# Kernel tuning notes

Measured on AMD Instinct MI355X. Metric: run time of the kernel, lower is better.

## Reference

```python
import math
import jax, jax.numpy as jnp
import numpy as np

N_GRAPHS = 400
N_PER = 50
N = N_GRAPHS * N_PER          # 20000 nodes
K = 12                        # k_neighbors
E = N * K                     # 240000 edges
ND = 128                      # node_dim
TD = 128                      # time_dim
LD = 128                      # latent_dim
SD = 32                       # species_emb_dim
L = 4                         # num_layers


def _lin(key, fi, fo):
    return (jax.random.normal(key, (fi, fo), dtype=jnp.float32) / np.sqrt(fi)).astype(jnp.float32)


def setup_inputs() -> dict:
    rng = np.random.default_rng(0)
    coords = (rng.standard_normal((N_GRAPHS, N_PER, 3)) * 3.0).astype(np.float32)
    # exact kNN per graph (loop=False): dst = center node, src = neighbor
    d = ((coords[:, :, None, :] - coords[:, None, :, :]) ** 2).sum(-1)  # [G, n, n]
    ii = np.arange(N_PER)
    d[:, ii, ii] = np.inf
    nbr = np.argpartition(d, K, axis=-1)[:, :, :K]                      # [G, n, K]
    base = (np.arange(N_GRAPHS) * N_PER)[:, None, None]
    edge_src = (nbr + base).reshape(-1).astype(np.int64)
    edge_dst = (np.broadcast_to(ii[None, :, None], (N_GRAPHS, N_PER, K)) + base).reshape(-1).astype(np.int64)
    batch_indices = np.repeat(np.arange(N_GRAPHS), N_PER).astype(np.int64)

    key = jax.random.key(0)
    ks = jax.random.split(key, 32)
    inp = {
        'z_nodes': jax.random.normal(ks[0], (N, LD), dtype=jnp.float32),
        't': jax.random.uniform(ks[1], (N_GRAPHS,), dtype=jnp.float32) * 1000.0,
        'cart_coords': jnp.asarray(coords.reshape(N, 3)),
        'species': jax.random.randint(ks[2], (N,), 1, 119),
        'batch_indices': jnp.asarray(batch_indices),
        'edge_src': jnp.asarray(edge_src),
        'edge_dst': jnp.asarray(edge_dst),
        # parameters
        'species_emb': jax.random.normal(ks[3], (119, SD), dtype=jnp.float32),
        'tm_W1': _lin(ks[4], TD, 2 * TD), 'tm_b1': jnp.zeros((2 * TD,), jnp.float32),
        'tm_W2': _lin(ks[5], 2 * TD, TD), 'tm_b2': jnp.zeros((TD,), jnp.float32),
        'ne_W': _lin(ks[6], LD + SD, ND), 'ne_b': jnp.zeros((ND,), jnp.float32),
        'eW1': jnp.stack([_lin(jax.random.fold_in(ks[7], l), 2 * ND + 1 + TD, ND) for l in range(L)]),
        'eb1': jnp.zeros((L, ND), jnp.float32),
        'eW2': jnp.stack([_lin(jax.random.fold_in(ks[8], l), ND, ND) for l in range(L)]),
        'eb2': jnp.zeros((L, ND), jnp.float32),
        'cW1': jnp.stack([_lin(jax.random.fold_in(ks[9], l), ND, ND) for l in range(L)]),
        'cb1': jnp.zeros((L, ND), jnp.float32),
        'cW2': jnp.stack([_lin(jax.random.fold_in(ks[10], l), ND, 1) for l in range(L)]),
        'nW1': jnp.stack([_lin(jax.random.fold_in(ks[11], l), 2 * ND + TD, ND) for l in range(L)]),
        'nb1': jnp.zeros((L, ND), jnp.float32),
        'nW2': jnp.stack([_lin(jax.random.fold_in(ks[12], l), ND, ND) for l in range(L)]),
        'nb2': jnp.zeros((L, ND), jnp.float32),
    }
    return inp


def reference(z_nodes, t, cart_coords, species, batch_indices, edge_src, edge_dst,
              species_emb, tm_W1, tm_b1, tm_W2, tm_b2, ne_W, ne_b,
              eW1, eb1, eW2, eb2, cW1, cb1, cW2, nW1, nb1, nW2, nb2):
    silu = jax.nn.silu
    # sinusoidal time embedding + time MLP
    half = TD // 2
    freqs = jnp.exp(jnp.arange(half, dtype=jnp.float32) * (-math.log(10000.0) / (half - 1)))
    ang = t[:, None] * freqs[None, :]                     # [G, half]
    temb = jnp.concatenate([jnp.sin(ang), jnp.cos(ang)], axis=-1)
    temb = silu(temb @ tm_W1 + tm_b1) @ tm_W2 + tm_b2     # [G, TD]
    t_nodes = temb[batch_indices]                         # [N, TD]

    sp = species_emb[species]                             # [N, SD]
    h = jnp.concatenate([z_nodes, sp], axis=-1) @ ne_W + ne_b  # [N, ND]

    diff = cart_coords[edge_src] - cart_coords[edge_dst]  # [E, 3]
    dist_sq = jnp.sum(diff * diff, axis=-1, keepdims=True)  # [E, 1]
    dist = jnp.sqrt(dist_sq + 1e-8)
    t_edges = t_nodes[edge_src]                           # [E, TD]

    n = h.shape[0]
    total_shift = jnp.zeros_like(cart_coords)
    for l in range(L):
        edge_in = jnp.concatenate([h[edge_src], h[edge_dst], dist_sq, t_edges], axis=-1)
        m = silu(edge_in @ eW1[l] + eb1[l])
        m = silu(m @ eW2[l] + eb2[l])                     # [E, ND]
        gate = silu(m @ cW1[l] + cb1[l]) @ cW2[l]         # [E, 1]
        shift = diff / dist * gate                        # [E, 3]
        total_shift = total_shift + jax.ops.segment_sum(shift, edge_dst, num_segments=n)
        m_i = jax.ops.segment_sum(m, edge_dst, num_segments=n)  # [N, ND]
        node_in = jnp.concatenate([h, m_i, t_nodes], axis=-1)
        h = h + (silu(node_in @ nW1[l] + nb1[l]) @ nW2[l] + nb2[l])
    return (total_shift, h)
```

## Files before the change

### kernel.cpp

```cpp
#include <hip/hip_runtime.h>
#include <math.h>

#define GN 400
#define NPER 50
#define NN 20000
#define LL 4

typedef __attribute__((ext_vector_type(8))) short short8;
typedef __attribute__((ext_vector_type(4))) float f32x4;

__device__ __forceinline__ float fast_rcp(float x) {
#if __has_builtin(__builtin_amdgcn_rcpf)
  return __builtin_amdgcn_rcpf(x);
#else
  return 1.0f / x;
#endif
}
__device__ __forceinline__ float silu_f(float x) {
  return x * fast_rcp(1.0f + __expf(-x));
}
__device__ __forceinline__ unsigned short f2bu(float f) {
  unsigned int u = __float_as_uint(f);
  unsigned int r = (u + 0x7fffu + ((u >> 16) & 1u)) >> 16;
  return (unsigned short)r;
}
__device__ __forceinline__ unsigned int pack2bf(float lo, float hi) {
  return (unsigned int)f2bu(lo) | ((unsigned int)f2bu(hi) << 16);
}
__device__ __forceinline__ float bhi(unsigned int u) { return __uint_as_float(u & 0xffff0000u); }
__device__ __forceinline__ float blo(unsigned int u) { return __uint_as_float(u << 16); }

__device__ __forceinline__ short8 pack8(const float* v) {
  union { unsigned int u[4]; short8 s; } t;
  t.u[0] = pack2bf(v[0], v[1]);
  t.u[1] = pack2bf(v[2], v[3]);
  t.u[2] = pack2bf(v[4], v[5]);
  t.u[3] = pack2bf(v[6], v[7]);
  return t.s;
}

__global__ __launch_bounds__(128) void time_kernel(
    const float* __restrict__ t,
    const float* __restrict__ tm_W1, const float* __restrict__ tm_b1,
    const float* __restrict__ tm_W2, const float* __restrict__ tm_b2,
    const float* __restrict__ eW1, const float* __restrict__ eb1,
    const float* __restrict__ nW1, const float* __restrict__ nb1,
    float* __restrict__ temb, float* __restrict__ tE, float* __restrict__ tN)
{
  int g = blockIdx.x;
  int j = threadIdx.x;
  __shared__ float x[128];
  __shared__ float hid[256];
  __shared__ float te[128];
  float tv = t[g];
  if (j < 64) {
    float f = __expf((float)j * (-9.210340371976184f / 63.0f));
    float a = tv * f;
    x[j] = sinf(a);
    x[j + 64] = cosf(a);
  }
  __syncthreads();
  for (int o = j; o < 256; o += 128) {
    float acc = tm_b1[o];
    for (int k = 0; k < 128; ++k) acc = fmaf(x[k], tm_W1[k * 256 + o], acc);
    hid[o] = silu_f(acc);
  }
  __syncthreads();
  {
    float acc = tm_b2[j];
    for (int k = 0; k < 256; ++k) acc = fmaf(hid[k], tm_W2[k * 128 + j], acc);
    te[j] = acc;
    temb[g * 128 + j] = acc;
  }
  __syncthreads();
  for (int l = 0; l < LL; ++l) {
    const float* W = eW1 + (l * 385 + 257) * 128;
    float acc = eb1[l * 128 + j];
    for (int k = 0; k < 128; ++k) acc = fmaf(te[k], W[k * 128 + j], acc);
    tE[(l * GN + g) * 128 + j] = acc;
    const float* Wn = nW1 + (l * 384 + 256) * 128;
    float acc2 = nb1[l * 128 + j];
    for (int k = 0; k < 128; ++k) acc2 = fmaf(te[k], Wn[k * 128 + j], acc2);
    tN[(l * GN + g) * 128 + j] = acc2;
  }
}

__global__ __launch_bounds__(256) void prep_transpose(
    const float* __restrict__ eW1, const float* __restrict__ eW2,
    const float* __restrict__ cW1, const float* __restrict__ nW1,
    const float* __restrict__ nW2, const float* __restrict__ ne_W,
    unsigned short* __restrict__ eABt, unsigned short* __restrict__ eW2t,
    unsigned short* __restrict__ cW1t, unsigned short* __restrict__ nW1t,
    unsigned short* __restrict__ nW2t, unsigned short* __restrict__ ne_Wt)
{
  __shared__ float tile[32][33];
  int j = blockIdx.y;
  const float* src;
  unsigned short* dst;
  int dstride = 128, Kj = 128;
  if (j < 28) {
    int l = j / 7, m = j % 7;
    switch (m) {
      case 0: src = eW1 + (l * 385 + 0) * 128;   dst = eABt + l * 256 * 128;             break;
      case 1: src = eW1 + (l * 385 + 128) * 128; dst = eABt + l * 256 * 128 + 128 * 128; break;
      case 2: src = eW2 + l * 16384;             dst = eW2t + l * 16384;                 break;
      case 3: src = cW1 + l * 16384;             dst = cW1t + l * 16384;                 break;
      case 4: src = nW1 + (l * 384 + 0) * 128;   dst = nW1t + l * 128 * 256; dstride = 256; break;
      case 5: src = nW1 + (l * 384 + 128) * 128; dst = nW1t + l * 128 * 256 + 128; dstride = 256; break;
      default: src = nW2 + l * 16384;            dst = nW2t + l * 16384;                 break;
    }
  } else {
    src = ne_W; dst = ne_Wt; dstride = 160; Kj = 160;
  }
  int gx = blockIdx.x;
  int tk = (gx % 5) * 32;
  int tn = (gx / 5) * 32;
  if (tk >= Kj) return;
  int ti = threadIdx.x >> 5, tj = threadIdx.x & 31;
#pragma unroll
  for (int p = 0; p < 4; ++p) {
    int i = ti + p * 8;
    tile[i][tj] = src[(tk + i) * 128 + tn + tj];
  }
  __syncthreads();
#pragma unroll
  for (int p = 0; p < 4; ++p) {
    int i = ti + p * 8;
    dst[(tn + i) * dstride + tk + tj] = f2bu(tile[tj][i]);
  }
}

__global__ __launch_bounds__(64) void edge_mfma(
    const unsigned short* __restrict__ hAB,
    const float* __restrict__ coords, const int* __restrict__ edge_src,
    const float* __restrict__ eW1,
    const unsigned short* __restrict__ eW2t, const float* __restrict__ eb2,
    const unsigned short* __restrict__ cW1t, const float* __restrict__ cb1,
    const float* __restrict__ cW2, const float* __restrict__ tE,
    unsigned short* __restrict__ m_i, float* __restrict__ shift_out,
    int l, int addflag)
{
  __shared__ unsigned short mbuf[48 * 136];
  __shared__ float sdir[48 * 4];
  __shared__ float sgate[48];

  int l6 = threadIdx.x;
  int e16 = l6 & 15, q = l6 >> 4;
  int nbase = blockIdx.x * 4;
  int ebase = blockIdx.x * 48;

  const unsigned short* eW2t_l = eW2t + l * 16384;
  const unsigned short* cW1t_l = cW1t + l * 16384;
  const float* eb2_l = eb2 + l * 128;
  const float* cb1_l = cb1 + l * 128;
  const float* cW2_l = cW2 + l * 128;
  const float* tE_l = tE + l * GN * 128;
  const float* wd = eW1 + (l * 385 + 256) * 128;

  int ssrc[3], sdst[3];
  float sds[3];
#pragma unroll
  for (int grp = 0; grp < 3; ++grp) {
    int eloc = grp * 16 + e16;
    int e = ebase + eloc;
    int src = edge_src[e];
    src = min(max(src, 0), NN - 1);
    int dst = nbase + eloc / 12;
    float dx = coords[src * 3 + 0] - coords[dst * 3 + 0];
    float dy = coords[src * 3 + 1] - coords[dst * 3 + 1];
    float dz = coords[src * 3 + 2] - coords[dst * 3 + 2];
    float ds = dx * dx + dy * dy + dz * dz;
    float rinv = 1.0f / sqrtf(ds + 1e-8f);
    if (q == 0) {
      sdir[eloc * 4 + 0] = dx * rinv;
      sdir[eloc * 4 + 1] = dy * rinv;
      sdir[eloc * 4 + 2] = dz * rinv;
    }
    ssrc[grp] = src; sdst[grp] = dst; sds[grp] = ds;
  }

  short8 bfr[3][4];
#pragma unroll
  for (int grp = 0; grp < 3; ++grp) {
    int g = sdst[grp] / NPER;
    float ds = sds[grp];
#pragma unroll
    for (int kc = 0; kc < 4; ++kc) {
      int k0 = kc * 32 + q * 8;
      uint4 ua = *(const uint4*)(hAB + ssrc[grp] * 256 + k0);
      uint4 ub = *(const uint4*)(hAB + sdst[grp] * 256 + 128 + k0);
      float4 w0 = *(const float4*)(wd + k0);
      float4 w1 = *(const float4*)(wd + k0 + 4);
      float4 t0 = *(const float4*)(tE_l + g * 128 + k0);
      float4 t1 = *(const float4*)(tE_l + g * 128 + k0 + 4);
      float v[8];
      v[0] = silu_f(blo(ua.x) + blo(ub.x) + ds * w0.x + t0.x);
      v[1] = silu_f(bhi(ua.x) + bhi(ub.x) + ds * w0.y + t0.y);
      v[2] = silu_f(blo(ua.y) + blo(ub.y) + ds * w0.z + t0.z);
      v[3] = silu_f(bhi(ua.y) + bhi(ub.y) + ds * w0.w + t0.w);
      v[4] = silu_f(blo(ua.z) + blo(ub.z) + ds * w1.x + t1.x);
      v[5] = silu_f(bhi(ua.z) + bhi(ub.z) + ds * w1.y + t1.y);
      v[6] = silu_f(blo(ua.w) + blo(ub.w) + ds * w1.z + t1.z);
      v[7] = silu_f(bhi(ua.w) + bhi(ub.w) + ds * w1.w + t1.w);
      bfr[grp][kc] = pack8(v);
    }
  }

#pragma unroll
  for (int mt = 0; mt < 8; ++mt) {
    short8 af[4];
#pragma unroll
    for (int kc = 0; kc < 4; ++kc)
      af[kc] = *(const short8*)(eW2t_l + (mt * 16 + e16) * 128 + kc * 32 + q * 8);
    f32x4 acc[3] = {(f32x4){0,0,0,0}, (f32x4){0,0,0,0}, (f32x4){0,0,0,0}};
#pragma unroll
    for (int kc = 0; kc < 4; ++kc) {
#pragma unroll
      for (int grp = 0; grp < 3; ++grp)
        acc[grp] = __builtin_amdgcn_mfma_f32_16x16x32_bf16(af[kc], bfr[grp][kc], acc[grp], 0, 0, 0);
    }
    float4 b4 = *(const float4*)(eb2_l + mt * 16 + q * 4);
#pragma unroll
    for (int grp = 0; grp < 3; ++grp) {
      float v0 = silu_f(acc[grp][0] + b4.x);
      float v1 = silu_f(acc[grp][1] + b4.y);
      float v2 = silu_f(acc[grp][2] + b4.z);
      float v3 = silu_f(acc[grp][3] + b4.w);
      uint2 p;
      p.x = pack2bf(v0, v1);
      p.y = pack2bf(v2, v3);
      *(uint2*)&mbuf[(grp * 16 + e16) * 136 + mt * 16 + q * 4] = p;
    }
  }
  __syncthreads();

  short8 af2[3][4];
#pragma unroll
  for (int grp = 0; grp < 3; ++grp)
#pragma unroll
    for (int kc = 0; kc < 4; ++kc)
      af2[grp][kc] = *(const short8*)&mbuf[(grp * 16 + e16) * 136 + kc * 32 + q * 8];

  float gp[3][4] = {{0,0,0,0},{0,0,0,0},{0,0,0,0}};
#pragma unroll
  for (int ct = 0; ct < 8; ++ct) {
    short8 bf[4];
#pragma unroll
    for (int kc = 0; kc < 4; ++kc)
      bf[kc] = *(const short8*)(cW1t_l + (ct * 16 + e16) * 128 + kc * 32 + q * 8);
    f32x4 acc[3] = {(f32x4){0,0,0,0}, (f32x4){0,0,0,0}, (f32x4){0,0,0,0}};
#pragma unroll
    for (int kc = 0; kc < 4; ++kc) {
#pragma unroll
      for (int grp = 0; grp < 3; ++grp)
        acc[grp] = __builtin_amdgcn_mfma_f32_16x16x32_bf16(af2[grp][kc], bf[kc], acc[grp], 0, 0, 0);
    }
    float cb = cb1_l[ct * 16 + e16];
    float c2 = cW2_l[ct * 16 + e16];
#pragma unroll
    for (int grp = 0; grp < 3; ++grp)
#pragma unroll
      for (int r = 0; r < 4; ++r)
        gp[grp][r] += silu_f(acc[grp][r] + cb) * c2;
  }
#pragma unroll
  for (int grp = 0; grp < 3; ++grp)
#pragma unroll
    for (int r = 0; r < 4; ++r) {
      float v = gp[grp][r];
      v += __shfl_xor(v, 1);
      v += __shfl_xor(v, 2);
      v += __shfl_xor(v, 4);
      v += __shfl_xor(v, 8);
      if (e16 == 0) sgate[grp * 16 + q * 4 + r] = v;
    }
  __syncthreads();

  {
    int nl = q, c8 = e16 * 8;
    float s[8] = {0,0,0,0,0,0,0,0};
#pragma unroll
    for (int r = 0; r < 12; ++r) {
      uint4 u = *(const uint4*)&mbuf[(nl * 12 + r) * 136 + c8];
      s[0] += blo(u.x); s[1] += bhi(u.x);
      s[2] += blo(u.y); s[3] += bhi(u.y);
      s[4] += blo(u.z); s[5] += bhi(u.z);
      s[6] += blo(u.w); s[7] += bhi(u.w);
    }
    uint4 o;
    o.x = pack2bf(s[0], s[1]); o.y = pack2bf(s[2], s[3]);
    o.z = pack2bf(s[4], s[5]); o.w = pack2bf(s[6], s[7]);
    *(uint4*)(m_i + (nbase + nl) * 128 + c8) = o;
  }
  if (l6 < 12) {
    int nl = l6 / 3, c = l6 - nl * 3;
    float s = 0.f;
#pragma unroll
    for (int r = 0; r < 12; ++r) {
      int e = nl * 12 + r;
      s = fmaf(sdir[e * 4 + c], sgate[e], s);
    }
    int n = nbase + nl;
    if (addflag) shift_out[n * 3 + c] += s;
    else         shift_out[n * 3 + c] = s;
  }
}

__global__ __launch_bounds__(64) void node_mfma(
    float* __restrict__ h, const unsigned short* __restrict__ m_i,
    const unsigned short* __restrict__ nW1t_l, const unsigned short* __restrict__ nW2t_l,
    const float* __restrict__ nb2_l, const float* __restrict__ tN_l,
    const unsigned short* __restrict__ eABt_next, unsigned short* __restrict__ hAB,
    int has_c)
{
  __shared__ unsigned short z1buf[16 * 136];
  __shared__ unsigned short hbuf[16 * 136];
  int l6 = threadIdx.x, e16 = l6 & 15, q = l6 >> 4;
  int row = blockIdx.x * 16 + e16;
  int g = row / NPER;

  short8 bfh[8];
#pragma unroll
  for (int kc = 0; kc < 8; ++kc) {
    int k0 = kc * 32 + q * 8;
    if (k0 < 128) {
      float4 f0 = *(const float4*)(h + row * 128 + k0);
      float4 f1 = *(const float4*)(h + row * 128 + k0 + 4);
      float v[8] = {f0.x, f0.y, f0.z, f0.w, f1.x, f1.y, f1.z, f1.w};
      bfh[kc] = pack8(v);
    } else {
      bfh[kc] = *(const short8*)(m_i + row * 128 + (k0 - 128));
    }
  }
#pragma unroll
  for (int mt = 0; mt < 8; ++mt) {
    short8 af[8];
#pragma unroll
    for (int kc = 0; kc < 8; ++kc)
      af[kc] = *(const short8*)(nW1t_l + (mt * 16 + e16) * 256 + kc * 32 + q * 8);
    f32x4 acc = (f32x4){0,0,0,0};
#pragma unroll
    for (int kc = 0; kc < 8; ++kc)
      acc = __builtin_amdgcn_mfma_f32_16x16x32_bf16(af[kc], bfh[kc], acc, 0, 0, 0);
    float4 tv = *(const float4*)(tN_l + g * 128 + mt * 16 + q * 4);
    float v0 = silu_f(acc[0] + tv.x);
    float v1 = silu_f(acc[1] + tv.y);
    float v2 = silu_f(acc[2] + tv.z);
    float v3 = silu_f(acc[3] + tv.w);
    uint2 p; p.x = pack2bf(v0, v1); p.y = pack2bf(v2, v3);
    *(uint2*)&z1buf[e16 * 136 + mt * 16 + q * 4] = p;
  }
  __syncthreads();

  short8 zf[4];
#pragma unroll
  for (int kc = 0; kc < 4; ++kc)
    zf[kc] = *(const short8*)&z1buf[e16 * 136 + kc * 32 + q * 8];
#pragma unroll
  for (int mt = 0; mt < 8; ++mt) {
    short8 af[4];
#pragma unroll
    for (int kc = 0; kc < 4; ++kc)
      af[kc] = *(const short8*)(nW2t_l + (mt * 16 + e16) * 128 + kc * 32 + q * 8);
    f32x4 acc = (f32x4){0,0,0,0};
#pragma unroll
    for (int kc = 0; kc < 4; ++kc)
      acc = __builtin_amdgcn_mfma_f32_16x16x32_bf16(af[kc], zf[kc], acc, 0, 0, 0);
    float4 hv = *(const float4*)(h + row * 128 + mt * 16 + q * 4);
    float4 b4 = *(const float4*)(nb2_l + mt * 16 + q * 4);
    float4 o;
    o.x = hv.x + acc[0] + b4.x;
    o.y = hv.y + acc[1] + b4.y;
    o.z = hv.z + acc[2] + b4.z;
    o.w = hv.w + acc[3] + b4.w;
    *(float4*)(h + row * 128 + mt * 16 + q * 4) = o;
    uint2 p; p.x = pack2bf(o.x, o.y); p.y = pack2bf(o.z, o.w);
    *(uint2*)&hbuf[e16 * 136 + mt * 16 + q * 4] = p;
  }
  if (has_c) {
    __syncthreads();
    short8 hf[4];
#pragma unroll
    for (int kc = 0; kc < 4; ++kc)
      hf[kc] = *(const short8*)&hbuf[e16 * 136 + kc * 32 + q * 8];
#pragma unroll
    for (int mt = 0; mt < 16; ++mt) {
      short8 af[4];
#pragma unroll
      for (int kc = 0; kc < 4; ++kc)
        af[kc] = *(const short8*)(eABt_next + (mt * 16 + e16) * 128 + kc * 32 + q * 8);
      f32x4 acc = (f32x4){0,0,0,0};
#pragma unroll
      for (int kc = 0; kc < 4; ++kc)
        acc = __builtin_amdgcn_mfma_f32_16x16x32_bf16(af[kc], hf[kc], acc, 0, 0, 0);
      uint2 p; p.x = pack2bf(acc[0], acc[1]); p.y = pack2bf(acc[2], acc[3]);
      *(uint2*)(hAB + row * 256 + mt * 16 + q * 4) = p;
    }
  }
}

__global__ __launch_bounds__(64) void encoder_mfma(
    const float* __restrict__ z, const int* __restrict__ species,
    const float* __restrict__ species_emb,
    const unsigned short* __restrict__ ne_Wt, const float* __restrict__ ne_b,
    const unsigned short* __restrict__ eABt0,
    float* __restrict__ h, unsigned short* __restrict__ hAB)
{
  __shared__ unsigned short hbuf[16 * 136];
  int l6 = threadIdx.x, e16 = l6 & 15, q = l6 >> 4;
  int row = blockIdx.x * 16 + e16;
  int sp = species[row];
  sp = min(max(sp, 0), 118);

  short8 bfh[5];
#pragma unroll
  for (int kc = 0; kc < 5; ++kc) {
    int k0 = kc * 32 + q * 8;
    const float* src = (k0 < 128) ? (z + row * 128 + k0)
                                  : (species_emb + sp * 32 + (k0 - 128));
    float4 f0 = *(const float4*)src;
    float4 f1 = *(const float4*)(src + 4);
    float v[8] = {f0.x, f0.y, f0.z, f0.w, f1.x, f1.y, f1.z, f1.w};
    bfh[kc] = pack8(v);
  }
#pragma unroll
  for (int mt = 0; mt < 8; ++mt) {
    short8 af[5];
#pragma unroll
    for (int kc = 0; kc < 5; ++kc)
      af[kc] = *(const short8*)(ne_Wt + (mt * 16 + e16) * 160 + kc * 32 + q * 8);
    f32x4 acc = (f32x4){0,0,0,0};
#pragma unroll
    for (int kc = 0; kc < 5; ++kc)
      acc = __builtin_amdgcn_mfma_f32_16x16x32_bf16(af[kc], bfh[kc], acc, 0, 0, 0);
    float4 b4 = *(const float4*)(ne_b + mt * 16 + q * 4);
    float4 o;
    o.x = acc[0] + b4.x; o.y = acc[1] + b4.y;
    o.z = acc[2] + b4.z; o.w = acc[3] + b4.w;
    *(float4*)(h + row * 128 + mt * 16 + q * 4) = o;
    uint2 p; p.x = pack2bf(o.x, o.y); p.y = pack2bf(o.z, o.w);
    *(uint2*)&hbuf[e16 * 136 + mt * 16 + q * 4] = p;
  }
  __syncthreads();
  short8 hf[4];
#pragma unroll
  for (int kc = 0; kc < 4; ++kc)
    hf[kc] = *(const short8*)&hbuf[e16 * 136 + kc * 32 + q * 8];
#pragma unroll
  for (int mt = 0; mt < 16; ++mt) {
    short8 af[4];
#pragma unroll
    for (int kc = 0; kc < 4; ++kc)
      af[kc] = *(const short8*)(eABt0 + (mt * 16 + e16) * 128 + kc * 32 + q * 8);
    f32x4 acc = (f32x4){0,0,0,0};
#pragma unroll
    for (int kc = 0; kc < 4; ++kc)
      acc = __builtin_amdgcn_mfma_f32_16x16x32_bf16(af[kc], hf[kc], acc, 0, 0, 0);
    uint2 p; p.x = pack2bf(acc[0], acc[1]); p.y = pack2bf(acc[2], acc[3]);
    *(uint2*)(hAB + row * 256 + mt * 16 + q * 4) = p;
  }
}

extern "C" void kernel_launch(void* const* d_in, const int* in_sizes, int n_in,
                              void* d_out, int out_size, void* d_ws, size_t ws_size,
                              hipStream_t stream)
{
  const float* z_nodes     = (const float*)d_in[0];
  const float* t           = (const float*)d_in[1];
  const float* coords      = (const float*)d_in[2];
  const int*   species     = (const int*)d_in[3];
  const int*   edge_src    = (const int*)d_in[5];
  const float* species_emb = (const float*)d_in[7];
  const float* tm_W1 = (const float*)d_in[8];
  const float* tm_b1 = (const float*)d_in[9];
  const float* tm_W2 = (const float*)d_in[10];
  const float* tm_b2 = (const float*)d_in[11];
  const float* ne_W  = (const float*)d_in[12];
  const float* ne_b  = (const float*)d_in[13];
  const float* eW1   = (const float*)d_in[14];
  const float* eb1   = (const float*)d_in[15];
  const float* eW2   = (const float*)d_in[16];
  const float* eb2   = (const float*)d_in[17];
  const float* cW1   = (const float*)d_in[18];
  const float* cb1   = (const float*)d_in[19];
  const float* cW2   = (const float*)d_in[20];
  const float* nW1   = (const float*)d_in[21];
  const float* nb1   = (const float*)d_in[22];
  const float* nW2   = (const float*)d_in[23];
  const float* nb2   = (const float*)d_in[24];

  char* wsb = (char*)d_ws;
  float* temb = (float*)(wsb + 0);
  float* tEb  = (float*)(wsb + 204800);
  float* tNb  = (float*)(wsb + 1024000);
  unsigned short* hAB  = (unsigned short*)(wsb + 1843200);
  unsigned short* m_i  = (unsigned short*)(wsb + 12083200);
  unsigned short* eABt = (unsigned short*)(wsb + 17203200);
  unsigned short* eW2t = (unsigned short*)(wsb + 17465344);
  unsigned short* cW1t = (unsigned short*)(wsb + 17596416);
  unsigned short* nW1t = (unsigned short*)(wsb + 17727488);
  unsigned short* nW2t = (unsigned short*)(wsb + 17989632);
  unsigned short* ne_Wt= (unsigned short*)(wsb + 18120704);

  float* outp  = (float*)d_out;
  float* shift = outp;
  float* h     = outp + 60000;

  time_kernel<<<GN, 128, 0, stream>>>(t, tm_W1, tm_b1, tm_W2, tm_b2,
                                      eW1, eb1, nW1, nb1, temb, tEb, tNb);
  prep_transpose<<<dim3(20, 29), 256, 0, stream>>>(eW1, eW2, cW1, nW1, nW2, ne_W,
                                                   eABt, eW2t, cW1t, nW1t, nW2t, ne_Wt);
  encoder_mfma<<<NN / 16, 64, 0, stream>>>(z_nodes, species, species_emb,
                                           ne_Wt, ne_b, eABt, h, hAB);
  for (int l = 0; l < LL; ++l) {
    edge_mfma<<<NN / 4, 64, 0, stream>>>(hAB, coords, edge_src, eW1,
                                         eW2t, eb2, cW1t, cb1, cW2, tEb,
                                         m_i, shift, l, (l > 0) ? 1 : 0);
    int has_c = (l < LL - 1) ? 1 : 0;
    node_mfma<<<NN / 16, 64, 0, stream>>>(h, m_i,
                                          nW1t + l * 128 * 256, nW2t + l * 16384,
                                          nb2 + l * 128, tNb + l * GN * 128,
                                          has_c ? (eABt + (l + 1) * 256 * 128) : eABt,
                                          hAB, has_c);
  }
}
```

Before: 550.3 us.

## Use two-wave blocks and cheaper bf16 packing across edge, node and encoder kernels

Edge blocks now hold two independent wavefronts, each with its own shared-memory slice, and the block-wide barriers are replaced by block memory fences. Node and encoder kernels split their output tiles across two waves so each wave does half the MFMA tiles. bf16 packing moves from round-to-nearest-even to add-and-perm rounding. The aim is higher occupancy, less barrier cost and fewer ALU ops. The risks are that intra-wave LDS reuse without a barrier depends on lockstep wavefront execution, that rounding changes slightly, and that the node and encoder kernels each do more redundant B-fragment loads per wave.

```diff
diff --git a/kernel.cpp b/kernel.cpp
--- a/kernel.cpp
+++ b/kernel.cpp
@@ -25,7 +25,13 @@
   return (unsigned short)r;
 }
 __device__ __forceinline__ unsigned int pack2bf(float lo, float hi) {
-  return (unsigned int)f2bu(lo) | ((unsigned int)f2bu(hi) << 16);
+  unsigned int a = __float_as_uint(lo) + 0x8000u;
+  unsigned int b = __float_as_uint(hi) + 0x8000u;
+#if __has_builtin(__builtin_amdgcn_perm)
+  return __builtin_amdgcn_perm(b, a, 0x07060302);
+#else
+  return (b & 0xffff0000u) | (a >> 16);
+#endif
 }
 __device__ __forceinline__ float bhi(unsigned int u) { return __uint_as_float(u & 0xffff0000u); }
 __device__ __forceinline__ float blo(unsigned int u) { return __uint_as_float(u << 16); }
@@ -130,7 +136,7 @@
   }
 }
 
-__global__ __launch_bounds__(64) void edge_mfma(
+__global__ __launch_bounds__(128) void edge_mfma(
     const unsigned short* __restrict__ hAB,
     const float* __restrict__ coords, const int* __restrict__ edge_src,
     const float* __restrict__ eW1,
@@ -140,14 +146,19 @@
     unsigned short* __restrict__ m_i, float* __restrict__ shift_out,
     int l, int addflag)
 {
-  __shared__ unsigned short mbuf[48 * 136];
-  __shared__ float sdir[48 * 4];
-  __shared__ float sgate[48];
-
-  int l6 = threadIdx.x;
+  __shared__ unsigned short mbuf[2][48 * 136];
+  __shared__ float sdir[2][48 * 4];
+  __shared__ float sgate[2][48];
+
+  int tid = threadIdx.x;
+  int wv = tid >> 6;
+  int l6 = tid & 63;
   int e16 = l6 & 15, q = l6 >> 4;
-  int nbase = blockIdx.x * 4;
-  int ebase = blockIdx.x * 48;
+  int nbase = blockIdx.x * 8 + wv * 4;
+  int ebase = nbase * 12;
+  unsigned short* mb = mbuf[wv];
+  float* sd = sdir[wv];
+  float* sg = sgate[wv];
 
   const unsigned short* eW2t_l = eW2t + l * 16384;
   const unsigned short* cW1t_l = cW1t + l * 16384;
@@ -172,9 +183,9 @@
     float ds = dx * dx + dy * dy + dz * dz;
     float rinv = 1.0f / sqrtf(ds + 1e-8f);
     if (q == 0) {
-      sdir[eloc * 4 + 0] = dx * rinv;
-      sdir[eloc * 4 + 1] = dy * rinv;
-      sdir[eloc * 4 + 2] = dz * rinv;
+      sd[eloc * 4 + 0] = dx * rinv;
+      sd[eloc * 4 + 1] = dy * rinv;
+      sd[eloc * 4 + 2] = dz * rinv;
     }
     ssrc[grp] = src; sdst[grp] = dst; sds[grp] = ds;
   }
@@ -229,17 +240,17 @@
       uint2 p;
       p.x = pack2bf(v0, v1);
       p.y = pack2bf(v2, v3);
-      *(uint2*)&mbuf[(grp * 16 + e16) * 136 + mt * 16 + q * 4] = p;
-    }
-  }
-  __syncthreads();
+      *(uint2*)&mb[(grp * 16 + e16) * 136 + mt * 16 + q * 4] = p;
+    }
+  }
+  __threadfence_block();
 
   short8 af2[3][4];
 #pragma unroll
   for (int grp = 0; grp < 3; ++grp)
 #pragma unroll
     for (int kc = 0; kc < 4; ++kc)
-      af2[grp][kc] = *(const short8*)&mbuf[(grp * 16 + e16) * 136 + kc * 32 + q * 8];
+      af2[grp][kc] = *(const short8*)&mb[(grp * 16 + e16) * 136 + kc * 32 + q * 8];
 
   float gp[3][4] = {{0,0,0,0},{0,0,0,0},{0,0,0,0}};
 #pragma unroll
@@ -272,16 +283,16 @@
       v += __shfl_xor(v, 2);
       v += __shfl_xor(v, 4);
       v += __shfl_xor(v, 8);
-      if (e16 == 0) sgate[grp * 16 + q * 4 + r] = v;
-    }
-  __syncthreads();
+      if (e16 == 0) sg[grp * 16 + q * 4 + r] = v;
+    }
+  __threadfence_block();
 
   {
     int nl = q, c8 = e16 * 8;
     float s[8] = {0,0,0,0,0,0,0,0};
 #pragma unroll
     for (int r = 0; r < 12; ++r) {
-      uint4 u = *(const uint4*)&mbuf[(nl * 12 + r) * 136 + c8];
+      uint4 u = *(const uint4*)&mb[(nl * 12 + r) * 136 + c8];
       s[0] += blo(u.x); s[1] += bhi(u.x);
       s[2] += blo(u.y); s[3] += bhi(u.y);
       s[4] += blo(u.z); s[5] += bhi(u.z);
@@ -298,7 +309,7 @@
 #pragma unroll
     for (int r = 0; r < 12; ++r) {
       int e = nl * 12 + r;
-      s = fmaf(sdir[e * 4 + c], sgate[e], s);
+      s = fmaf(sd[e * 4 + c], sg[e], s);
     }
     int n = nbase + nl;
     if (addflag) shift_out[n * 3 + c] += s;
@@ -306,7 +317,7 @@
   }
 }
 
-__global__ __launch_bounds__(64) void node_mfma(
+__global__ __launch_bounds__(128) void node_mfma(
     float* __restrict__ h, const unsigned short* __restrict__ m_i,
     const unsigned short* __restrict__ nW1t_l, const unsigned short* __restrict__ nW2t_l,
     const float* __restrict__ nb2_l, const float* __restrict__ tN_l,
@@ -315,7 +326,9 @@
 {
   __shared__ unsigned short z1buf[16 * 136];
   __shared__ unsigned short hbuf[16 * 136];
-  int l6 = threadIdx.x, e16 = l6 & 15, q = l6 >> 4;
+  int tid = threadIdx.x;
+  int wv = tid >> 6, l6 = tid & 63;
+  int e16 = l6 & 15, q = l6 >> 4;
   int row = blockIdx.x * 16 + e16;
   int g = row / NPER;
 
@@ -333,7 +346,8 @@
     }
   }
 #pragma unroll
-  for (int mt = 0; mt < 8; ++mt) {
+  for (int mi = 0; mi < 4; ++mi) {
+    int mt = wv * 4 + mi;
     short8 af[8];
 #pragma unroll
     for (int kc = 0; kc < 8; ++kc)
@@ -357,7 +371,8 @@
   for (int kc = 0; kc < 4; ++kc)
     zf[kc] = *(const short8*)&z1buf[e16 * 136 + kc * 32 + q * 8];
 #pragma unroll
-  for (int mt = 0; mt < 8; ++mt) {
+  for (int mi = 0; mi < 4; ++mi) {
+    int mt = wv * 4 + mi;
     short8 af[4];
 #pragma unroll
     for (int kc = 0; kc < 4; ++kc)
@@ -384,7 +399,8 @@
     for (int kc = 0; kc < 4; ++kc)
       hf[kc] = *(const short8*)&hbuf[e16 * 136 + kc * 32 + q * 8];
 #pragma unroll
-    for (int mt = 0; mt < 16; ++mt) {
+    for (int mi = 0; mi < 8; ++mi) {
+      int mt = wv * 8 + mi;
       short8 af[4];
 #pragma unroll
       for (int kc = 0; kc < 4; ++kc)
@@ -399,7 +415,7 @@
   }
 }
 
-__global__ __launch_bounds__(64) void encoder_mfma(
+__global__ __launch_bounds__(128) void encoder_mfma(
     const float* __restrict__ z, const int* __restrict__ species,
     const float* __restrict__ species_emb,
     const unsigned short* __restrict__ ne_Wt, const float* __restrict__ ne_b,
@@ -407,7 +423,9 @@
     float* __restrict__ h, unsigned short* __restrict__ hAB)
 {
   __shared__ unsigned short hbuf[16 * 136];
-  int l6 = threadIdx.x, e16 = l6 & 15, q = l6 >> 4;
+  int tid = threadIdx.x;
+  int wv = tid >> 6, l6 = tid & 63;
+  int e16 = l6 & 15, q = l6 >> 4;
   int row = blockIdx.x * 16 + e16;
   int sp = species[row];
   sp = min(max(sp, 0), 118);
@@ -424,7 +442,8 @@
     bfh[kc] = pack8(v);
   }
 #pragma unroll
-  for (int mt = 0; mt < 8; ++mt) {
+  for (int mi = 0; mi < 4; ++mi) {
+    int mt = wv * 4 + mi;
     short8 af[5];
 #pragma unroll
     for (int kc = 0; kc < 5; ++kc)
@@ -447,7 +466,8 @@
   for (int kc = 0; kc < 4; ++kc)
     hf[kc] = *(const short8*)&hbuf[e16 * 136 + kc * 32 + q * 8];
 #pragma unroll
-  for (int mt = 0; mt < 16; ++mt) {
+  for (int mi = 0; mi < 8; ++mi) {
+    int mt = wv * 8 + mi;
     short8 af[4];
 #pragma unroll
     for (int kc = 0; kc < 4; ++kc)
@@ -510,17 +530,17 @@
                                       eW1, eb1, nW1, nb1, temb, tEb, tNb);
   prep_transpose<<<dim3(20, 29), 256, 0, stream>>>(eW1, eW2, cW1, nW1, nW2, ne_W,
                                                    eABt, eW2t, cW1t, nW1t, nW2t, ne_Wt);
-  encoder_mfma<<<NN / 16, 64, 0, stream>>>(z_nodes, species, species_emb,
-                                           ne_Wt, ne_b, eABt, h, hAB);
+  encoder_mfma<<<NN / 16, 128, 0, stream>>>(z_nodes, species, species_emb,
+                                            ne_Wt, ne_b, eABt, h, hAB);
   for (int l = 0; l < LL; ++l) {
-    edge_mfma<<<NN / 4, 64, 0, stream>>>(hAB, coords, edge_src, eW1,
-                                         eW2t, eb2, cW1t, cb1, cW2, tEb,
-                                         m_i, shift, l, (l > 0) ? 1 : 0);
+    edge_mfma<<<NN / 8, 128, 0, stream>>>(hAB, coords, edge_src, eW1,
+                                          eW2t, eb2, cW1t, cb1, cW2, tEb,
+                                          m_i, shift, l, (l > 0) ? 1 : 0);
     int has_c = (l < LL - 1) ? 1 : 0;
-    node_mfma<<<NN / 16, 64, 0, stream>>>(h, m_i,
-                                          nW1t + l * 128 * 256, nW2t + l * 16384,
-                                          nb2 + l * 128, tNb + l * GN * 128,
-                                          has_c ? (eABt + (l + 1) * 256 * 128) : eABt,
-                                          hAB, has_c);
-  }
-}
+    node_mfma<<<NN / 16, 128, 0, stream>>>(h, m_i,
+                                           nW1t + l * 128 * 256, nW2t + l * 16384,
+                                           nb2 + l * 128, tNb + l * GN * 128,
+                                           has_c ? (eABt + (l + 1) * 256 * 128) : eABt,
+                                           hAB, has_c);
+  }
+}
```

Result: no change. 554.8 us (+0.8%).

## Process eight nodes per edge block to reuse weight fragments; cheaper bf16 packing

Applied to the files above, without the earlier changes.

Each edge_mfma block now handles two 48-edge chunks (8 destination nodes), so each eW2/cW1 weight fragment loaded from global memory feeds twice as many MFMAs. The grid is halved and shared memory is doubled. Separately, pack2bf now rounds half-up and packs the two values with a byte-permute instruction instead of round-to-nearest-even. This cuts instruction count but changes the rounding slightly. The larger register footprint (bfr, af2 and accumulators all doubled) risks spills or lower occupancy.

```diff
diff --git a/kernel.cpp b/kernel.cpp
--- a/kernel.cpp
+++ b/kernel.cpp
@@ -25,7 +25,13 @@
   return (unsigned short)r;
 }
 __device__ __forceinline__ unsigned int pack2bf(float lo, float hi) {
-  return (unsigned int)f2bu(lo) | ((unsigned int)f2bu(hi) << 16);
+  unsigned int a = __float_as_uint(lo) + 0x8000u;
+  unsigned int b = __float_as_uint(hi) + 0x8000u;
+#if __has_builtin(__builtin_amdgcn_perm)
+  return __builtin_amdgcn_perm(b, a, 0x07060302);
+#else
+  return (b & 0xffff0000u) | (a >> 16);
+#endif
 }
 __device__ __forceinline__ float bhi(unsigned int u) { return __uint_as_float(u & 0xffff0000u); }
 __device__ __forceinline__ float blo(unsigned int u) { return __uint_as_float(u << 16); }
@@ -140,14 +146,13 @@
     unsigned short* __restrict__ m_i, float* __restrict__ shift_out,
     int l, int addflag)
 {
-  __shared__ unsigned short mbuf[48 * 136];
-  __shared__ float sdir[48 * 4];
-  __shared__ float sgate[48];
+  __shared__ unsigned short mbuf[2][48 * 136];
+  __shared__ float sdir[2][48 * 4];
+  __shared__ float sgate[2][48];
 
   int l6 = threadIdx.x;
   int e16 = l6 & 15, q = l6 >> 4;
-  int nbase = blockIdx.x * 4;
-  int ebase = blockIdx.x * 48;
+  int nbase0 = blockIdx.x * 8;
 
   const unsigned short* eW2t_l = eW2t + l * 16384;
   const unsigned short* cW1t_l = cW1t + l * 16384;
@@ -157,38 +162,45 @@
   const float* tE_l = tE + l * GN * 128;
   const float* wd = eW1 + (l * 385 + 256) * 128;
 
-  int ssrc[3], sdst[3];
-  float sds[3];
+  int ssrc[2][3], sdst[2][3];
+  float sds[2][3];
+#pragma unroll
+  for (int c = 0; c < 2; ++c) {
+    int nbase = nbase0 + c * 4;
+    int ebase = nbase * 12;
+#pragma unroll
+    for (int grp = 0; grp < 3; ++grp) {
+      int eloc = grp * 16 + e16;
+      int e = ebase + eloc;
+      int src = edge_src[e];
+      src = min(max(src, 0), NN - 1);
+      int dst = nbase + eloc / 12;
+      float dx = coords[src * 3 + 0] - coords[dst * 3 + 0];
+      float dy = coords[src * 3 + 1] - coords[dst * 3 + 1];
+      float dz = coords[src * 3 + 2] - coords[dst * 3 + 2];
+      float ds = dx * dx + dy * dy + dz * dz;
+      float rinv = 1.0f / sqrtf(ds + 1e-8f);
+      if (q == 0) {
+        sdir[c][eloc * 4 + 0] = dx * rinv;
+        sdir[c][eloc * 4 + 1] = dy * rinv;
+        sdir[c][eloc * 4 + 2] = dz * rinv;
+      }
+      ssrc[c][grp] = src; sdst[c][grp] = dst; sds[c][grp] = ds;
+    }
+  }
+
+  short8 bfr[2][3][4];
+#pragma unroll
+  for (int c = 0; c < 2; ++c)
 #pragma unroll
   for (int grp = 0; grp < 3; ++grp) {
-    int eloc = grp * 16 + e16;
-    int e = ebase + eloc;
-    int src = edge_src[e];
-    src = min(max(src, 0), NN - 1);
-    int dst = nbase + eloc / 12;
-    float dx = coords[src * 3 + 0] - coords[dst * 3 + 0];
-    float dy = coords[src * 3 + 1] - coords[dst * 3 + 1];
-    float dz = coords[src * 3 + 2] - coords[dst * 3 + 2];
-    float ds = dx * dx + dy * dy + dz * dz;
-    float rinv = 1.0f / sqrtf(ds + 1e-8f);
-    if (q == 0) {
-      sdir[eloc * 4 + 0] = dx * rinv;
-      sdir[eloc * 4 + 1] = dy * rinv;
-      sdir[eloc * 4 + 2] = dz * rinv;
-    }
-    ssrc[grp] = src; sdst[grp] = dst; sds[grp] = ds;
-  }
-
-  short8 bfr[3][4];
-#pragma unroll
-  for (int grp = 0; grp < 3; ++grp) {
-    int g = sdst[grp] / NPER;
-    float ds = sds[grp];
+    int g = sdst[c][grp] / NPER;
+    float ds = sds[c][grp];
 #pragma unroll
     for (int kc = 0; kc < 4; ++kc) {
       int k0 = kc * 32 + q * 8;
-      uint4 ua = *(const uint4*)(hAB + ssrc[grp] * 256 + k0);
-      uint4 ub = *(const uint4*)(hAB + sdst[grp] * 256 + 128 + k0);
+      uint4 ua = *(const uint4*)(hAB + ssrc[c][grp] * 256 + k0);
+      uint4 ub = *(const uint4*)(hAB + sdst[c][grp] * 256 + 128 + k0);
       float4 w0 = *(const float4*)(wd + k0);
       float4 w1 = *(const float4*)(wd + k0 + 4);
       float4 t0 = *(const float4*)(tE_l + g * 128 + k0);
@@ -202,7 +214,7 @@
       v[5] = silu_f(bhi(ua.z) + bhi(ub.z) + ds * w1.y + t1.y);
       v[6] = silu_f(blo(ua.w) + blo(ub.w) + ds * w1.z + t1.z);
       v[7] = silu_f(bhi(ua.w) + bhi(ub.w) + ds * w1.w + t1.w);
-      bfr[grp][kc] = pack8(v);
+      bfr[c][grp][kc] = pack8(v);
     }
   }
 
@@ -212,76 +224,96 @@
 #pragma unroll
     for (int kc = 0; kc < 4; ++kc)
       af[kc] = *(const short8*)(eW2t_l + (mt * 16 + e16) * 128 + kc * 32 + q * 8);
-    f32x4 acc[3] = {(f32x4){0,0,0,0}, (f32x4){0,0,0,0}, (f32x4){0,0,0,0}};
-#pragma unroll
-    for (int kc = 0; kc < 4; ++kc) {
-#pragma unroll
-      for (int grp = 0; grp < 3; ++grp)
-        acc[grp] = __builtin_amdgcn_mfma_f32_16x16x32_bf16(af[kc], bfr[grp][kc], acc[grp], 0, 0, 0);
-    }
+    f32x4 acc[2][3];
+#pragma unroll
+    for (int c = 0; c < 2; ++c)
+#pragma unroll
+      for (int grp = 0; grp < 3; ++grp) acc[c][grp] = (f32x4){0, 0, 0, 0};
+#pragma unroll
+    for (int kc = 0; kc < 4; ++kc)
+#pragma unroll
+      for (int c = 0; c < 2; ++c)
+#pragma unroll
+        for (int grp = 0; grp < 3; ++grp)
+          acc[c][grp] = __builtin_amdgcn_mfma_f32_16x16x32_bf16(af[kc], bfr[c][grp][kc], acc[c][grp], 0, 0, 0);
     float4 b4 = *(const float4*)(eb2_l + mt * 16 + q * 4);
 #pragma unroll
-    for (int grp = 0; grp < 3; ++grp) {
-      float v0 = silu_f(acc[grp][0] + b4.x);
-      float v1 = silu_f(acc[grp][1] + b4.y);
-      float v2 = silu_f(acc[grp][2] + b4.z);
-      float v3 = silu_f(acc[grp][3] + b4.w);
-      uint2 p;
-      p.x = pack2bf(v0, v1);
-      p.y = pack2bf(v2, v3);
-      *(uint2*)&mbuf[(grp * 16 + e16) * 136 + mt * 16 + q * 4] = p;
-    }
-  }
-  __syncthreads();
-
-  short8 af2[3][4];
-#pragma unroll
-  for (int grp = 0; grp < 3; ++grp)
-#pragma unroll
-    for (int kc = 0; kc < 4; ++kc)
-      af2[grp][kc] = *(const short8*)&mbuf[(grp * 16 + e16) * 136 + kc * 32 + q * 8];
-
-  float gp[3][4] = {{0,0,0,0},{0,0,0,0},{0,0,0,0}};
+    for (int c = 0; c < 2; ++c)
+#pragma unroll
+      for (int grp = 0; grp < 3; ++grp) {
+        float v0 = silu_f(acc[c][grp][0] + b4.x);
+        float v1 = silu_f(acc[c][grp][1] + b4.y);
+        float v2 = silu_f(acc[c][grp][2] + b4.z);
+        float v3 = silu_f(acc[c][grp][3] + b4.w);
+        uint2 p;
+        p.x = pack2bf(v0, v1);
+        p.y = pack2bf(v2, v3);
+        *(uint2*)&mbuf[c][(grp * 16 + e16) * 136 + mt * 16 + q * 4] = p;
+      }
+  }
+  __syncthreads();
+
+  short8 af2[2][3][4];
+#pragma unroll
+  for (int c = 0; c < 2; ++c)
+#pragma unroll
+    for (int grp = 0; grp < 3; ++grp)
+#pragma unroll
+      for (int kc = 0; kc < 4; ++kc)
+        af2[c][grp][kc] = *(const short8*)&mbuf[c][(grp * 16 + e16) * 136 + kc * 32 + q * 8];
+
+  float gp[2][3][4] = {{{0,0,0,0},{0,0,0,0},{0,0,0,0}},
+                       {{0,0,0,0},{0,0,0,0},{0,0,0,0}}};
 #pragma unroll
   for (int ct = 0; ct < 8; ++ct) {
     short8 bf[4];
 #pragma unroll
     for (int kc = 0; kc < 4; ++kc)
       bf[kc] = *(const short8*)(cW1t_l + (ct * 16 + e16) * 128 + kc * 32 + q * 8);
-    f32x4 acc[3] = {(f32x4){0,0,0,0}, (f32x4){0,0,0,0}, (f32x4){0,0,0,0}};
-#pragma unroll
-    for (int kc = 0; kc < 4; ++kc) {
-#pragma unroll
-      for (int grp = 0; grp < 3; ++grp)
-        acc[grp] = __builtin_amdgcn_mfma_f32_16x16x32_bf16(af2[grp][kc], bf[kc], acc[grp], 0, 0, 0);
-    }
+    f32x4 acc[2][3];
+#pragma unroll
+    for (int c = 0; c < 2; ++c)
+#pragma unroll
+      for (int grp = 0; grp < 3; ++grp) acc[c][grp] = (f32x4){0, 0, 0, 0};
+#pragma unroll
+    for (int kc = 0; kc < 4; ++kc)
+#pragma unroll
+      for (int c = 0; c < 2; ++c)
+#pragma unroll
+        for (int grp = 0; grp < 3; ++grp)
+          acc[c][grp] = __builtin_amdgcn_mfma_f32_16x16x32_bf16(af2[c][grp][kc], bf[kc], acc[c][grp], 0, 0, 0);
     float cb = cb1_l[ct * 16 + e16];
     float c2 = cW2_l[ct * 16 + e16];
 #pragma unroll
+    for (int c = 0; c < 2; ++c)
+#pragma unroll
+      for (int grp = 0; grp < 3; ++grp)
+#pragma unroll
+        for (int r = 0; r < 4; ++r)
+          gp[c][grp][r] += silu_f(acc[c][grp][r] + cb) * c2;
+  }
+#pragma unroll
+  for (int c = 0; c < 2; ++c)
+#pragma unroll
     for (int grp = 0; grp < 3; ++grp)
 #pragma unroll
-      for (int r = 0; r < 4; ++r)
-        gp[grp][r] += silu_f(acc[grp][r] + cb) * c2;
-  }
-#pragma unroll
-  for (int grp = 0; grp < 3; ++grp)
-#pragma unroll
-    for (int r = 0; r < 4; ++r) {
-      float v = gp[grp][r];
-      v += __shfl_xor(v, 1);
-      v += __shfl_xor(v, 2);
-      v += __shfl_xor(v, 4);
-      v += __shfl_xor(v, 8);
-      if (e16 == 0) sgate[grp * 16 + q * 4 + r] = v;
-    }
-  __syncthreads();
-
-  {
+      for (int r = 0; r < 4; ++r) {
+        float v = gp[c][grp][r];
+        v += __shfl_xor(v, 1);
+        v += __shfl_xor(v, 2);
+        v += __shfl_xor(v, 4);
+        v += __shfl_xor(v, 8);
+        if (e16 == 0) sgate[c][grp * 16 + q * 4 + r] = v;
+      }
+  __syncthreads();
+
+#pragma unroll
+  for (int c = 0; c < 2; ++c) {
     int nl = q, c8 = e16 * 8;
     float s[8] = {0,0,0,0,0,0,0,0};
 #pragma unroll
     for (int r = 0; r < 12; ++r) {
-      uint4 u = *(const uint4*)&mbuf[(nl * 12 + r) * 136 + c8];
+      uint4 u = *(const uint4*)&mbuf[c][(nl * 12 + r) * 136 + c8];
       s[0] += blo(u.x); s[1] += bhi(u.x);
       s[2] += blo(u.y); s[3] += bhi(u.y);
       s[4] += blo(u.z); s[5] += bhi(u.z);
@@ -290,19 +322,20 @@
     uint4 o;
     o.x = pack2bf(s[0], s[1]); o.y = pack2bf(s[2], s[3]);
     o.z = pack2bf(s[4], s[5]); o.w = pack2bf(s[6], s[7]);
-    *(uint4*)(m_i + (nbase + nl) * 128 + c8) = o;
-  }
-  if (l6 < 12) {
-    int nl = l6 / 3, c = l6 - nl * 3;
+    *(uint4*)(m_i + (nbase0 + c * 4 + nl) * 128 + c8) = o;
+  }
+  if (l6 < 24) {
+    int nl8 = l6 / 3, comp = l6 - nl8 * 3;
+    int c = nl8 >> 2, nl = nl8 & 3;
     float s = 0.f;
 #pragma unroll
     for (int r = 0; r < 12; ++r) {
       int e = nl * 12 + r;
-      s = fmaf(sdir[e * 4 + c], sgate[e], s);
-    }
-    int n = nbase + nl;
-    if (addflag) shift_out[n * 3 + c] += s;
-    else         shift_out[n * 3 + c] = s;
+      s = fmaf(sdir[c][e * 4 + comp], sgate[c][e], s);
+    }
+    int n = nbase0 + c * 4 + nl;
+    if (addflag) shift_out[n * 3 + comp] += s;
+    else         shift_out[n * 3 + comp] = s;
   }
 }
 
@@ -513,7 +546,7 @@
   encoder_mfma<<<NN / 16, 64, 0, stream>>>(z_nodes, species, species_emb,
                                            ne_Wt, ne_b, eABt, h, hAB);
   for (int l = 0; l < LL; ++l) {
-    edge_mfma<<<NN / 4, 64, 0, stream>>>(hAB, coords, edge_src, eW1,
+    edge_mfma<<<NN / 8, 64, 0, stream>>>(hAB, coords, edge_src, eW1,
                                          eW2t, eb2, cW1t, cb1, cW2, tEb,
                                          m_i, shift, l, (l > 0) ? 1 : 0);
     int has_c = (l < LL - 1) ? 1 : 0;
```

Measured after the change: 609.7 us. 10.8% more time.

## Split node and encoder output tiles across four waves; cheapen bf16 packing

Applied to the files above, without the earlier changes.

The node and encoder MFMA kernels now launch 256 threads per 16-row block, and each of the four waves computes a quarter of the output column tiles instead of one wave doing all of them. This raises parallelism per block and cuts the serial MFMA chain each wave runs. The bf16 pack helper switches from round-to-nearest-even to round-half-up with a byte permute, which saves ALU work but changes rounding on ties. Each wave still loads the full input fragments redundantly.

```diff
diff --git a/kernel.cpp b/kernel.cpp
--- a/kernel.cpp
+++ b/kernel.cpp
@@ -25,7 +25,13 @@
   return (unsigned short)r;
 }
 __device__ __forceinline__ unsigned int pack2bf(float lo, float hi) {
-  return (unsigned int)f2bu(lo) | ((unsigned int)f2bu(hi) << 16);
+  unsigned int a = __float_as_uint(lo) + 0x8000u;
+  unsigned int b = __float_as_uint(hi) + 0x8000u;
+#if __has_builtin(__builtin_amdgcn_perm)
+  return __builtin_amdgcn_perm(b, a, 0x07060302);
+#else
+  return (b & 0xffff0000u) | (a >> 16);
+#endif
 }
 __device__ __forceinline__ float bhi(unsigned int u) { return __uint_as_float(u & 0xffff0000u); }
 __device__ __forceinline__ float blo(unsigned int u) { return __uint_as_float(u << 16); }
@@ -306,7 +312,7 @@
   }
 }
 
-__global__ __launch_bounds__(64) void node_mfma(
+__global__ __launch_bounds__(256) void node_mfma(
     float* __restrict__ h, const unsigned short* __restrict__ m_i,
     const unsigned short* __restrict__ nW1t_l, const unsigned short* __restrict__ nW2t_l,
     const float* __restrict__ nb2_l, const float* __restrict__ tN_l,
@@ -315,7 +321,9 @@
 {
   __shared__ unsigned short z1buf[16 * 136];
   __shared__ unsigned short hbuf[16 * 136];
-  int l6 = threadIdx.x, e16 = l6 & 15, q = l6 >> 4;
+  int tid = threadIdx.x;
+  int wv = tid >> 6, l6 = tid & 63;
+  int e16 = l6 & 15, q = l6 >> 4;
   int row = blockIdx.x * 16 + e16;
   int g = row / NPER;
 
@@ -333,7 +341,8 @@
     }
   }
 #pragma unroll
-  for (int mt = 0; mt < 8; ++mt) {
+  for (int mi = 0; mi < 2; ++mi) {
+    int mt = wv * 2 + mi;
     short8 af[8];
 #pragma unroll
     for (int kc = 0; kc < 8; ++kc)
@@ -357,7 +366,8 @@
   for (int kc = 0; kc < 4; ++kc)
     zf[kc] = *(const short8*)&z1buf[e16 * 136 + kc * 32 + q * 8];
 #pragma unroll
-  for (int mt = 0; mt < 8; ++mt) {
+  for (int mi = 0; mi < 2; ++mi) {
+    int mt = wv * 2 + mi;
     short8 af[4];
 #pragma unroll
     for (int kc = 0; kc < 4; ++kc)
@@ -384,7 +394,8 @@
     for (int kc = 0; kc < 4; ++kc)
       hf[kc] = *(const short8*)&hbuf[e16 * 136 + kc * 32 + q * 8];
 #pragma unroll
-    for (int mt = 0; mt < 16; ++mt) {
+    for (int mi = 0; mi < 4; ++mi) {
+      int mt = wv * 4 + mi;
       short8 af[4];
 #pragma unroll
       for (int kc = 0; kc < 4; ++kc)
@@ -399,7 +410,7 @@
   }
 }
 
-__global__ __launch_bounds__(64) void encoder_mfma(
+__global__ __launch_bounds__(256) void encoder_mfma(
     const float* __restrict__ z, const int* __restrict__ species,
     const float* __restrict__ species_emb,
     const unsigned short* __restrict__ ne_Wt, const float* __restrict__ ne_b,
@@ -407,7 +418,9 @@
     float* __restrict__ h, unsigned short* __restrict__ hAB)
 {
   __shared__ unsigned short hbuf[16 * 136];
-  int l6 = threadIdx.x, e16 = l6 & 15, q = l6 >> 4;
+  int tid = threadIdx.x;
+  int wv = tid >> 6, l6 = tid & 63;
+  int e16 = l6 & 15, q = l6 >> 4;
   int row = blockIdx.x * 16 + e16;
   int sp = species[row];
   sp = min(max(sp, 0), 118);
@@ -424,7 +437,8 @@
     bfh[kc] = pack8(v);
   }
 #pragma unroll
-  for (int mt = 0; mt < 8; ++mt) {
+  for (int mi = 0; mi < 2; ++mi) {
+    int mt = wv * 2 + mi;
     short8 af[5];
 #pragma unroll
     for (int kc = 0; kc < 5; ++kc)
@@ -447,7 +461,8 @@
   for (int kc = 0; kc < 4; ++kc)
     hf[kc] = *(const short8*)&hbuf[e16 * 136 + kc * 32 + q * 8];
 #pragma unroll
-  for (int mt = 0; mt < 16; ++mt) {
+  for (int mi = 0; mi < 4; ++mi) {
+    int mt = wv * 4 + mi;
     short8 af[4];
 #pragma unroll
     for (int kc = 0; kc < 4; ++kc)
@@ -510,17 +525,17 @@
                                       eW1, eb1, nW1, nb1, temb, tEb, tNb);
   prep_transpose<<<dim3(20, 29), 256, 0, stream>>>(eW1, eW2, cW1, nW1, nW2, ne_W,
                                                    eABt, eW2t, cW1t, nW1t, nW2t, ne_Wt);
-  encoder_mfma<<<NN / 16, 64, 0, stream>>>(z_nodes, species, species_emb,
-                                           ne_Wt, ne_b, eABt, h, hAB);
+  encoder_mfma<<<NN / 16, 256, 0, stream>>>(z_nodes, species, species_emb,
+                                            ne_Wt, ne_b, eABt, h, hAB);
   for (int l = 0; l < LL; ++l) {
     edge_mfma<<<NN / 4, 64, 0, stream>>>(hAB, coords, edge_src, eW1,
                                          eW2t, eb2, cW1t, cb1, cW2, tEb,
                                          m_i, shift, l, (l > 0) ? 1 : 0);
     int has_c = (l < LL - 1) ? 1 : 0;
-    node_mfma<<<NN / 16, 64, 0, stream>>>(h, m_i,
-                                          nW1t + l * 128 * 256, nW2t + l * 16384,
-                                          nb2 + l * 128, tNb + l * GN * 128,
-                                          has_c ? (eABt + (l + 1) * 256 * 128) : eABt,
-                                          hAB, has_c);
-  }
-}
+    node_mfma<<<NN / 16, 256, 0, stream>>>(h, m_i,
+                                           nW1t + l * 128 * 256, nW2t + l * 16384,
+                                           nb2 + l * 128, tNb + l * GN * 128,
+                                           has_c ? (eABt + (l + 1) * 256 * 128) : eABt,
+                                           hAB, has_c);
+  }
+}
```

Result: slower. 573.6 us (+4.2%).
